# Optimization experiments

Measured on AMD Instinct MI355X. Metric: run time of the kernel, lower is better.

Reference implementation:

```python
import jax, jax.numpy as jnp
import numpy as np

BOND_D = 4    # disentangler bond dim (hard-coded 4 in torch init)
BOND_I = 16   # isometry bond dim (bond_dim kwarg)
F = 2         # feature_dim = 2*nCh, nCh=1 -> [x, 1-x] embedding
LEVELS = [128, 64, 32, 16, 8, 4]
NUM_CLASSES = 10
BATCH = 16


def setup_inputs() -> dict:
    key = jax.random.key(0)
    ks = iter(jax.random.split(key, 128))
    inp = {}
    inp["x"] = jax.random.uniform(next(ks), (BATCH, 1, 128, 128), dtype=jnp.float32)

    def mps_params(P, D, O):
        A = 0.2 * jax.random.normal(next(ks), (P, 4, F, D, D), dtype=jnp.float32)
        v = 0.2 * jax.random.normal(next(ks), (P, D), dtype=jnp.float32)
        w = 0.2 * jax.random.normal(next(ks), (P, D, O), dtype=jnp.float32)
        return A, v, w

    for l, H in enumerate(LEVELS, start=1):
        Pd = ((H - 2) // 2) ** 2   # number of disentangler patches
        Pi = (H // 2) ** 2         # number of isometry patches
        inp[f"d{l}A"], inp[f"d{l}v"], inp[f"d{l}w"] = mps_params(Pd, BOND_D, 4)
        inp[f"i{l}A"], inp[f"i{l}v"], inp[f"i{l}w"] = mps_params(Pi, BOND_I, 1)
    inp["fA"], inp["fv"], inp["fw"] = mps_params(1, BOND_I, NUM_CLASSES)
    return inp


def _patches(x):
    # x: [b, H, W] (H, W even) -> [b, (H/2)*(W/2), 4], same site order as
    # torch unfold(2,2,2).unfold(3,2,2).reshape(..., 4)
    b, H, W = x.shape
    return x.reshape(b, H // 2, 2, W // 2, 2).transpose(0, 1, 3, 2, 4).reshape(b, -1, 4)


def _unpatch(y, nh, nw):
    # y: [b, nh*nw, 4] -> [b, 2*nh, 2*nw], inverse spatial placement of 2x2 blocks
    b = y.shape[0]
    return y.reshape(b, nh, nw, 2, 2).transpose(0, 1, 3, 2, 4).reshape(b, 2 * nh, 2 * nw)


def _mps(patches, A, v, w):
    # Batched per-patch ReLU-MPS over 4 sites.
    # patches [b,P,4], A [P,4,F,D,D], v [P,D], w [P,D,O] -> [b,P,O]
    phi = jnp.stack([patches, 1.0 - patches], axis=-1)          # [b,P,4,F]
    M = jnp.einsum('bpsf,psfij->bpsij', phi, A)                 # [b,P,4,D,D]
    vec = jnp.einsum('pi,bpij->bpj', v, M[:, :, 0])             # [b,P,D]
    for s in range(1, 4):
        vec = jnp.einsum('bpi,bpij->bpj', vec, M[:, :, s])
    return jax.nn.relu(jnp.einsum('bpi,pio->bpo', vec, w))


def _level(x, dA, dv, dw, iA, iv, iw):
    # One MERA layer: disentangle shifted interior patches, write back, then
    # isometry-pool the full grid 2x2 -> 1.
    b, H, W = x.shape
    nh = (H - 2) // 2
    y = _mps(_patches(x[:, 1:-1, 1:-1]), dA, dv, dw)            # [b, nh*nh, 4]
    x = x.at[:, 1:-1, 1:-1].set(_unpatch(y, nh, nh))
    y2 = _mps(_patches(x), iA, iv, iw)                          # [b, (H/2)^2, 1]
    return y2.reshape(b, H // 2, W // 2)


def reference(x, d1A, d1v, d1w, i1A, i1v, i1w,
              d2A, d2v, d2w, i2A, i2v, i2w,
              d3A, d3v, d3w, i3A, i3v, i3w,
              d4A, d4v, d4w, i4A, i4v, i4w,
              d5A, d5v, d5w, i5A, i5v, i5w,
              d6A, d6v, d6w, i6A, i6v, i6w,
              fA, fv, fw):
    h = x[:, 0]  # nCh = 1
    levels = [(d1A, d1v, d1w, i1A, i1v, i1w), (d2A, d2v, d2w, i2A, i2v, i2w),
              (d3A, d3v, d3w, i3A, i3v, i3w), (d4A, d4v, d4w, i4A, i4v, i4w),
              (d5A, d5v, d5w, i5A, i5v, i5w), (d6A, d6v, d6w, i6A, i6v, i6w)]
    for p in levels:
        h = _level(h, *p)
    flat = h.reshape(h.shape[0], 1, 4)         # final 2x2 grid -> 4 sites
    return _mps(flat, fA, fv, fw)[:, 0]        # [b, NUM_CLASSES]
```

## Files before the change

### kernel.cpp

```cpp
#include <hip/hip_runtime.h>

#define BATCH 16

template <int CTRL>
__device__ __forceinline__ float qperm(float x) {
  int xi = __float_as_int(x);
  return __int_as_float(__builtin_amdgcn_update_dpp(xi, xi, CTRL, 0xF, 0xF, true));
}

__device__ __forceinline__ float4 f4fma(float s, float4 a, float4 c) {
  c.x = fmaf(s, a.x, c.x);
  c.y = fmaf(s, a.y, c.y);
  c.z = fmaf(s, a.z, c.z);
  c.w = fmaf(s, a.w, c.w);
  return c;
}

__device__ __forceinline__ void mps16_chain(const float* A, int jq,
                                            const float tt[4], float vec[4]) {
#pragma unroll
  for (int s = 0; s < 4; s++) {
    const float4* A0v = (const float4*)(A + s * 512) + jq;
    const float4* A1v = A0v + 64;
    float4 q0 = {0.f, 0.f, 0.f, 0.f}, q1 = {0.f, 0.f, 0.f, 0.f};
#define ISTEP(i)                                         \
  {                                                      \
    float sv = qperm<(((i) >> 2) * 0x55)>(vec[(i) & 3]); \
    q0 = f4fma(sv, A0v[(i) * 4], q0);                    \
    q1 = f4fma(sv, A1v[(i) * 4], q1);                    \
  }
    ISTEP(0) ISTEP(1) ISTEP(2) ISTEP(3)
    ISTEP(4) ISTEP(5) ISTEP(6) ISTEP(7)
    ISTEP(8) ISTEP(9) ISTEP(10) ISTEP(11)
    ISTEP(12) ISTEP(13) ISTEP(14) ISTEP(15)
#undef ISTEP
    float ph = tt[s], om = 1.0f - ph;
    vec[0] = ph * q0.x + om * q1.x;
    vec[1] = ph * q0.y + om * q1.y;
    vec[2] = ph * q0.z + om * q1.z;
    vec[3] = ph * q0.w + om * q1.w;
  }
}

template <int H, int XS>
__device__ __forceinline__ float fused_di_quad(
    const float* __restrict__ xb, int p, int jq,
    const float* __restrict__ dA, const float* __restrict__ dv,
    const float* __restrict__ dw,
    const float* __restrict__ iA, const float* __restrict__ iv,
    const float* __restrict__ iw) {
  constexpr int NH = (H - 2) / 2;
  constexpr int W2 = H / 2;
  int pi = p / W2, pj = p % W2;
  int r = 2 * pi + (jq >> 1), c = 2 * pj + (jq & 1);
  float tcell;
  bool border = (r == 0) | (r == H - 1) | (c == 0) | (c == H - 1);
  if (border) {
    tcell = xb[(r * H + c) * XS];
  } else {
    int dpi = (r - 1) >> 1, dpj = (c - 1) >> 1;
    int sd = ((r - 1) & 1) * 2 + ((c - 1) & 1);
    int dp = dpi * NH + dpj;
    int R0 = 1 + 2 * dpi, C0 = 1 + 2 * dpj;
    float tins[4];
    tins[0] = xb[(R0 * H + C0) * XS];
    tins[1] = xb[(R0 * H + C0 + 1) * XS];
    tins[2] = xb[((R0 + 1) * H + C0) * XS];
    tins[3] = xb[((R0 + 1) * H + C0 + 1) * XS];
    const float4* Av = (const float4*)(dA + dp * 128);
    float4 dvv = *(const float4*)(dv + dp * 4);
    float v0 = dvv.x, v1 = dvv.y, v2 = dvv.z, v3 = dvv.w;
#pragma unroll
    for (int s = 0; s < 4; s++) {
      const float4* A0 = Av + s * 8;
      float4 q0 = {0.f, 0.f, 0.f, 0.f}, q1 = {0.f, 0.f, 0.f, 0.f};
      q0 = f4fma(v0, A0[0], q0);
      q0 = f4fma(v1, A0[1], q0);
      q0 = f4fma(v2, A0[2], q0);
      q0 = f4fma(v3, A0[3], q0);
      q1 = f4fma(v0, A0[4], q1);
      q1 = f4fma(v1, A0[5], q1);
      q1 = f4fma(v2, A0[6], q1);
      q1 = f4fma(v3, A0[7], q1);
      float ph = tins[s], om = 1.0f - ph;
      v0 = ph * q0.x + om * q1.x;
      v1 = ph * q0.y + om * q1.y;
      v2 = ph * q0.z + om * q1.z;
      v3 = ph * q0.w + om * q1.w;
    }
    const float* wp = dw + dp * 16 + sd;
    float y = v0 * wp[0];
    y = fmaf(v1, wp[4], y);
    y = fmaf(v2, wp[8], y);
    y = fmaf(v3, wp[12], y);
    tcell = fmaxf(y, 0.0f);
  }
  float tt[4];
  tt[0] = qperm<0x00>(tcell);
  tt[1] = qperm<0x55>(tcell);
  tt[2] = qperm<0xAA>(tcell);
  tt[3] = qperm<0xFF>(tcell);
  float4 vv = *(const float4*)(iv + p * 16 + 4 * jq);
  float vec[4] = {vv.x, vv.y, vv.z, vv.w};
  mps16_chain(iA + (size_t)p * 2048, jq, tt, vec);
  float4 wv = *(const float4*)(iw + p * 16 + 4 * jq);
  float partial = vec[0] * wv.x;
  partial = fmaf(vec[1], wv.y, partial);
  partial = fmaf(vec[2], wv.z, partial);
  partial = fmaf(vec[3], wv.w, partial);
  partial += qperm<0xB1>(partial);
  partial += qperm<0x4E>(partial);
  return fmaxf(partial, 0.0f);
}

#define OFF_IA 0
#define OFF_IV 8192
#define OFF_IW 8256
#define OFF_DA 8320
#define OFF_DV 9640
#define OFF_DW 9680
#define LDS_TOT 9840

template <int H>
__global__ __launch_bounds__(256) void level_kernel(
    const float* __restrict__ xT, float* __restrict__ hn,
    const float* __restrict__ dA, const float* __restrict__ dv,
    const float* __restrict__ dw, const float* __restrict__ iA,
    const float* __restrict__ iv, const float* __restrict__ iw) {
  constexpr int W2 = H / 2, NH = (H - 2) / 2;
  __shared__ __align__(16) float lds[LDS_TOT];
  float4* l4 = (float4*)lds;
  const int tid = threadIdx.x;
  const int p0 = blockIdx.x * 4;
  const int pi = p0 / W2, pj0 = p0 % W2;
  const int jq = tid & 3, b = (tid >> 2) & 15, w = tid >> 6;
  const int pj = pj0 + w;
  const int r = 2 * pi + (jq >> 1), c = 2 * pj + (jq & 1);
  const bool border = (r == 0) | (r == H - 1) | (c == 0) | (c == H - 1);
  const int dpi = (r - 1) >> 1, dpj = (c - 1) >> 1;

  float xv0, xv1, xv2, xv3;
  if (border) {
    xv0 = xT[(r * H + c) * 16 + b];
  } else {
    int R0 = 1 + 2 * dpi, C0 = 1 + 2 * dpj;
    xv0 = xT[(R0 * H + C0) * 16 + b];
    xv1 = xT[(R0 * H + C0 + 1) * 16 + b];
    xv2 = xT[((R0 + 1) * H + C0) * 16 + b];
    xv3 = xT[((R0 + 1) * H + C0 + 1) * 16 + b];
  }

  {
    const float4* iA4 = (const float4*)iA + p0 * 512;
    float4 ra[8];
#pragma unroll
    for (int k = 0; k < 8; k++) ra[k] = iA4[tid + k * 256];

    float4 rd0, rd1;
    int sl0, gr0, sl1, gr1;
    const bool md1 = tid < 64;
    {
      int g = tid;
      int rs = g / 160, rem = g % 160, cs = rem / 32;
      gr0 = rem % 32;
      int di = min(max(pi - 1 + rs, 0), NH - 1);
      int dj = min(max(pj0 - 1 + cs, 0), NH - 1);
      sl0 = rs * 5 + cs;
      rd0 = *((const float4*)dA + (di * NH + dj) * 32 + gr0);
    }
    if (md1) {
      int g = tid + 256;
      int rs = g / 160, rem = g % 160, cs = rem / 32;
      gr1 = rem % 32;
      int di = min(max(pi - 1 + rs, 0), NH - 1);
      int dj = min(max(pj0 - 1 + cs, 0), NH - 1);
      sl1 = rs * 5 + cs;
      rd1 = *((const float4*)dA + (di * NH + dj) * 32 + gr1);
    }
    float4 rv;
    const bool mv = tid < 10;
    if (mv) {
      int rs = tid / 5, cs = tid % 5;
      int di = min(max(pi - 1 + rs, 0), NH - 1);
      int dj = min(max(pj0 - 1 + cs, 0), NH - 1);
      rv = *((const float4*)dv + (di * NH + dj));
    }
    float4 rw;
    const bool mw = tid < 40;
    if (mw) {
      int rs = tid / 20, rem = tid % 20, cs = rem / 4, gr = rem % 4;
      int di = min(max(pi - 1 + rs, 0), NH - 1);
      int dj = min(max(pj0 - 1 + cs, 0), NH - 1);
      rw = *((const float4*)dw + (di * NH + dj) * 4 + gr);
    }
    float4 rvv, rww;
    const bool mi = tid < 16;
    if (mi) {
      rvv = *((const float4*)iv + p0 * 4 + tid);
      rww = *((const float4*)iw + p0 * 4 + tid);
    }
#pragma unroll
    for (int k = 0; k < 8; k++) l4[OFF_IA / 4 + tid + k * 256] = ra[k];
    l4[OFF_DA / 4 + sl0 * 33 + gr0] = rd0;
    if (md1) l4[OFF_DA / 4 + sl1 * 33 + gr1] = rd1;
    if (mv) l4[OFF_DV / 4 + tid] = rv;
    if (mw) l4[OFF_DW / 4 + tid] = rw;
    if (mi) l4[OFF_IV / 4 + tid] = rvv;
    if (mi) l4[OFF_IW / 4 + tid] = rww;
  }
  __syncthreads();

  float tcell;
  if (border) {
    tcell = xv0;
  } else {
    int sd = ((r - 1) & 1) * 2 + ((c - 1) & 1);
    int slot = (dpi - pi + 1) * 5 + (dpj - pj0 + 1);
    const float4* Av = (const float4*)(lds + OFF_DA + slot * 132);
    float4 dvv = *(const float4*)(lds + OFF_DV + slot * 4);
    float v0 = dvv.x, v1 = dvv.y, v2 = dvv.z, v3 = dvv.w;
    float tins[4] = {xv0, xv1, xv2, xv3};
#pragma unroll
    for (int s = 0; s < 4; s++) {
      const float4* A0 = Av + s * 8;
      float4 q0 = {0.f, 0.f, 0.f, 0.f}, q1 = {0.f, 0.f, 0.f, 0.f};
      q0 = f4fma(v0, A0[0], q0);
      q0 = f4fma(v1, A0[1], q0);
      q0 = f4fma(v2, A0[2], q0);
      q0 = f4fma(v3, A0[3], q0);
      q1 = f4fma(v0, A0[4], q1);
      q1 = f4fma(v1, A0[5], q1);
      q1 = f4fma(v2, A0[6], q1);
      q1 = f4fma(v3, A0[7], q1);
      float ph = tins[s], om = 1.0f - ph;
      v0 = ph * q0.x + om * q1.x;
      v1 = ph * q0.y + om * q1.y;
      v2 = ph * q0.z + om * q1.z;
      v3 = ph * q0.w + om * q1.w;
    }
    const float* wp = lds + OFF_DW + slot * 16 + sd;
    float y = v0 * wp[0];
    y = fmaf(v1, wp[4], y);
    y = fmaf(v2, wp[8], y);
    y = fmaf(v3, wp[12], y);
    tcell = fmaxf(y, 0.0f);
  }
  float tt[4];
  tt[0] = qperm<0x00>(tcell);
  tt[1] = qperm<0x55>(tcell);
  tt[2] = qperm<0xAA>(tcell);
  tt[3] = qperm<0xFF>(tcell);
  float4 vv = *(const float4*)(lds + OFF_IV + w * 16 + 4 * jq);
  float vec[4] = {vv.x, vv.y, vv.z, vv.w};
  mps16_chain(lds + OFF_IA + w * 2048, jq, tt, vec);
  float4 wv = *(const float4*)(lds + OFF_IW + w * 16 + 4 * jq);
  float partial = vec[0] * wv.x;
  partial = fmaf(vec[1], wv.y, partial);
  partial = fmaf(vec[2], wv.z, partial);
  partial = fmaf(vec[3], wv.w, partial);
  partial += qperm<0xB1>(partial);
  partial += qperm<0x4E>(partial);
  if (jq == 0) hn[(p0 + w) * 16 + b] = fmaxf(partial, 0.0f);
}

__global__ __launch_bounds__(256) void transpose_kernel(
    const float* __restrict__ x, float* __restrict__ xT) {
  __shared__ float t[64][17];
  int tid = threadIdx.x;
  int c0 = blockIdx.x * 64;
  {
    int bb = tid >> 4, c4 = tid & 15;
    float4 v = *((const float4*)(x + bb * 16384 + c0) + c4);
    t[c4 * 4 + 0][bb] = v.x;
    t[c4 * 4 + 1][bb] = v.y;
    t[c4 * 4 + 2][bb] = v.z;
    t[c4 * 4 + 3][bb] = v.w;
  }
  __syncthreads();
  {
    int cl = tid >> 2, bq = tid & 3;
    float4 v;
    v.x = t[cl][bq * 4 + 0];
    v.y = t[cl][bq * 4 + 1];
    v.z = t[cl][bq * 4 + 2];
    v.w = t[cl][bq * 4 + 3];
    *((float4*)(xT + (c0 + cl) * 16) + bq) = v;
  }
}

struct TailArgs {
  const float* h4;
  const float* in[15];
  float* out;
};

__global__ __launch_bounds__(256) void tail2_kernel(TailArgs a) {
  __shared__ float h5l[4][16];
  __shared__ float h6l[4][4];
  int tid = threadIdx.x;
  {
    int jq = tid & 3, p = (tid >> 2) & 15, bl = tid >> 6;
    int b = blockIdx.x * 4 + bl;
    float o = fused_di_quad<8, 16>(a.h4 + b, p, jq, a.in[0], a.in[1], a.in[2],
                                   a.in[3], a.in[4], a.in[5]);
    if (jq == 0) h5l[bl][p] = o;
  }
  __syncthreads();
  if (tid < 64) {
    int jq = tid & 3, p = (tid >> 2) & 3, bl = tid >> 4;
    float o = fused_di_quad<4, 1>(&h5l[bl][0], p, jq, a.in[6], a.in[7],
                                  a.in[8], a.in[9], a.in[10], a.in[11]);
    if (jq == 0) h6l[bl][p] = o;
  }
  __syncthreads();
  if (tid < 16) {
    int jq = tid & 3, bl = tid >> 2;
    const float* fA = a.in[12];
    const float* fv = a.in[13];
    const float* fw = a.in[14];
    float tt[4] = {h6l[bl][0], h6l[bl][1], h6l[bl][2], h6l[bl][3]};
    float4 vv = *(const float4*)(fv + 4 * jq);
    float vec[4] = {vv.x, vv.y, vv.z, vv.w};
    mps16_chain(fA, jq, tt, vec);
    float acc[10];
#pragma unroll
    for (int o = 0; o < 10; o++) acc[o] = 0.f;
#pragma unroll
    for (int k = 0; k < 4; k++)
#pragma unroll
      for (int o = 0; o < 10; o++)
        acc[o] = fmaf(vec[k], fw[(4 * jq + k) * 10 + o], acc[o]);
#pragma unroll
    for (int o = 0; o < 10; o++) {
      acc[o] += qperm<0xB1>(acc[o]);
      acc[o] += qperm<0x4E>(acc[o]);
    }
    if (jq == 0) {
      int b = blockIdx.x * 4 + bl;
#pragma unroll
      for (int o = 0; o < 10; o++) a.out[b * 10 + o] = fmaxf(acc[o], 0.0f);
    }
  }
}

extern "C" void kernel_launch(void* const* d_in, const int* in_sizes, int n_in,
                              void* d_out, int out_size, void* d_ws, size_t ws_size,
                              hipStream_t stream) {
  const float* x = (const float*)d_in[0];
  float* ws = (float*)d_ws;
  float* xT = ws;
  float* h1 = xT + 262144;
  float* h2 = h1 + 65536;
  float* h3 = h2 + 16384;
  float* h4 = h3 + 4096;

  transpose_kernel<<<256, 256, 0, stream>>>(x, xT);
  level_kernel<128><<<1024, 256, 0, stream>>>(
      xT, h1, (const float*)d_in[1], (const float*)d_in[2],
      (const float*)d_in[3], (const float*)d_in[4], (const float*)d_in[5],
      (const float*)d_in[6]);
  level_kernel<64><<<256, 256, 0, stream>>>(
      h1, h2, (const float*)d_in[7], (const float*)d_in[8],
      (const float*)d_in[9], (const float*)d_in[10], (const float*)d_in[11],
      (const float*)d_in[12]);
  level_kernel<32><<<64, 256, 0, stream>>>(
      h2, h3, (const float*)d_in[13], (const float*)d_in[14],
      (const float*)d_in[15], (const float*)d_in[16], (const float*)d_in[17],
      (const float*)d_in[18]);
  level_kernel<16><<<16, 256, 0, stream>>>(
      h3, h4, (const float*)d_in[19], (const float*)d_in[20],
      (const float*)d_in[21], (const float*)d_in[22], (const float*)d_in[23],
      (const float*)d_in[24]);

  TailArgs ta;
  ta.h4 = h4;
  for (int i = 0; i < 15; i++) ta.in[i] = (const float*)d_in[25 + i];
  ta.out = (float*)d_out;
  tail2_kernel<<<4, 256, 0, stream>>>(ta);
}
```

Before: 195.5 us.

## Fuse all MERA levels into one cooperative persistent kernel with grid syncs

Replaces the transpose kernel, four per-level kernels and the tail kernel with one cooperative kernel of 512 blocks that runs each level as a phase separated by grid.sync. Level 1 reads the raw input layout directly, which drops the transpose pass, and each block handles two patch groups. Level 5 moves out of the tail into its own phase, and the tail stages its weights in LDS inside a single block. This removes per-launch overhead and inter-kernel gaps, at the cost of grid-wide barriers, idle blocks in the late phases, and uncoalesced strided reads of the raw input in level 1.

```diff
diff --git a/kernel.cpp b/kernel.cpp
--- a/kernel.cpp
+++ b/kernel.cpp
@@ -1,4 +1,7 @@
 #include <hip/hip_runtime.h>
+#include <hip/hip_cooperative_groups.h>
+
+namespace cg = cooperative_groups;
 
 #define BATCH 16
 
@@ -44,11 +47,8 @@
 
 template <int H, int XS>
 __device__ __forceinline__ float fused_di_quad(
-    const float* __restrict__ xb, int p, int jq,
-    const float* __restrict__ dA, const float* __restrict__ dv,
-    const float* __restrict__ dw,
-    const float* __restrict__ iA, const float* __restrict__ iv,
-    const float* __restrict__ iw) {
+    const float* xb, int p, int jq, const float* dA, const float* dv,
+    const float* dw, const float* iA, const float* iv, const float* iw) {
   constexpr int NH = (H - 2) / 2;
   constexpr int W2 = H / 2;
   int pi = p / W2, pj = p % W2;
@@ -120,18 +120,21 @@
 #define OFF_DV 9640
 #define OFF_DW 9680
 #define LDS_TOT 9840
-
-template <int H>
-__global__ __launch_bounds__(256) void level_kernel(
-    const float* __restrict__ xT, float* __restrict__ hn,
-    const float* __restrict__ dA, const float* __restrict__ dv,
-    const float* __restrict__ dw, const float* __restrict__ iA,
-    const float* __restrict__ iv, const float* __restrict__ iw) {
+#define OFF_X6 (OFF_DA + 264)
+#define OFF_H6 (OFF_DA + 1056)
+
+template <int H, bool RAW>
+__device__ void level_phase(float* lds, const float* __restrict__ xin,
+                            float* __restrict__ hn,
+                            const float* __restrict__ dA,
+                            const float* __restrict__ dv,
+                            const float* __restrict__ dw,
+                            const float* __restrict__ iA,
+                            const float* __restrict__ iv,
+                            const float* __restrict__ iw, int p0) {
   constexpr int W2 = H / 2, NH = (H - 2) / 2;
-  __shared__ __align__(16) float lds[LDS_TOT];
   float4* l4 = (float4*)lds;
   const int tid = threadIdx.x;
-  const int p0 = blockIdx.x * 4;
   const int pi = p0 / W2, pj0 = p0 % W2;
   const int jq = tid & 3, b = (tid >> 2) & 15, w = tid >> 6;
   const int pj = pj0 + w;
@@ -140,15 +143,30 @@
   const int dpi = (r - 1) >> 1, dpj = (c - 1) >> 1;
 
   float xv0, xv1, xv2, xv3;
-  if (border) {
-    xv0 = xT[(r * H + c) * 16 + b];
+  if (RAW) {
+    const float* xb = xin + b * H * H;
+    if (border) {
+      xv0 = xb[r * H + c];
+    } else {
+      int R0 = 1 + 2 * dpi, C0 = 1 + 2 * dpj;
+      xv0 = xb[R0 * H + C0];
+      xv1 = xb[R0 * H + C0 + 1];
+      xv2 = xb[(R0 + 1) * H + C0];
+      xv3 = xb[(R0 + 1) * H + C0 + 1];
+    }
   } else {
-    int R0 = 1 + 2 * dpi, C0 = 1 + 2 * dpj;
-    xv0 = xT[(R0 * H + C0) * 16 + b];
-    xv1 = xT[(R0 * H + C0 + 1) * 16 + b];
-    xv2 = xT[((R0 + 1) * H + C0) * 16 + b];
-    xv3 = xT[((R0 + 1) * H + C0 + 1) * 16 + b];
-  }
+    if (border) {
+      xv0 = xin[(r * H + c) * 16 + b];
+    } else {
+      int R0 = 1 + 2 * dpi, C0 = 1 + 2 * dpj;
+      xv0 = xin[(R0 * H + C0) * 16 + b];
+      xv1 = xin[(R0 * H + C0 + 1) * 16 + b];
+      xv2 = xin[((R0 + 1) * H + C0) * 16 + b];
+      xv3 = xin[((R0 + 1) * H + C0 + 1) * 16 + b];
+    }
+  }
+
+  __syncthreads();
 
   {
     const float4* iA4 = (const float4*)iA + p0 * 512;
@@ -263,65 +281,85 @@
   if (jq == 0) hn[(p0 + w) * 16 + b] = fmaxf(partial, 0.0f);
 }
 
-__global__ __launch_bounds__(256) void transpose_kernel(
-    const float* __restrict__ x, float* __restrict__ xT) {
-  __shared__ float t[64][17];
-  int tid = threadIdx.x;
-  int c0 = blockIdx.x * 64;
-  {
-    int bb = tid >> 4, c4 = tid & 15;
-    float4 v = *((const float4*)(x + bb * 16384 + c0) + c4);
-    t[c4 * 4 + 0][bb] = v.x;
-    t[c4 * 4 + 1][bb] = v.y;
-    t[c4 * 4 + 2][bb] = v.z;
-    t[c4 * 4 + 3][bb] = v.w;
-  }
-  __syncthreads();
-  {
-    int cl = tid >> 2, bq = tid & 3;
-    float4 v;
-    v.x = t[cl][bq * 4 + 0];
-    v.y = t[cl][bq * 4 + 1];
-    v.z = t[cl][bq * 4 + 2];
-    v.w = t[cl][bq * 4 + 3];
-    *((float4*)(xT + (c0 + cl) * 16) + bq) = v;
-  }
-}
-
-struct TailArgs {
-  const float* h4;
-  const float* in[15];
+struct MegaArgs {
+  const float* x;
+  const float* P[39];
+  float* h1;
+  float* h2;
+  float* h3;
+  float* h4;
+  float* h5;
   float* out;
 };
 
-__global__ __launch_bounds__(256) void tail2_kernel(TailArgs a) {
-  __shared__ float h5l[4][16];
-  __shared__ float h6l[4][4];
-  int tid = threadIdx.x;
+__device__ void tail_phase(float* lds, const MegaArgs& a) {
+  float4* l4 = (float4*)lds;
+  const int tid = threadIdx.x;
+  const float* d6A = a.P[30];
+  const float* d6v = a.P[31];
+  const float* d6w = a.P[32];
+  const float* i6A = a.P[33];
+  const float* i6v = a.P[34];
+  const float* i6w = a.P[35];
+  const float* fA = a.P[36];
+  const float* fv = a.P[37];
+  const float* fw = a.P[38];
+  __syncthreads();
   {
-    int jq = tid & 3, p = (tid >> 2) & 15, bl = tid >> 6;
-    int b = blockIdx.x * 4 + bl;
-    float o = fused_di_quad<8, 16>(a.h4 + b, p, jq, a.in[0], a.in[1], a.in[2],
-                                   a.in[3], a.in[4], a.in[5]);
-    if (jq == 0) h5l[bl][p] = o;
+    const float4* g = (const float4*)i6A;
+    float4 ra[8];
+#pragma unroll
+    for (int k = 0; k < 8; k++) ra[k] = g[tid + k * 256];
+    float4 rdA;
+    const bool mA = tid < 32;
+    if (mA) rdA = ((const float4*)d6A)[tid];
+    float4 rdv;
+    const bool mdv = tid == 0;
+    if (mdv) rdv = ((const float4*)d6v)[0];
+    float4 rdw;
+    const bool mdw = tid < 4;
+    if (mdw) rdw = ((const float4*)d6w)[tid];
+    float4 riv, riw;
+    const bool mi = tid < 16;
+    if (mi) {
+      riv = ((const float4*)i6v)[tid];
+      riw = ((const float4*)i6w)[tid];
+    }
+    float x6v = a.h5[(tid & 15) * 16 + (tid >> 4)];
+#pragma unroll
+    for (int k = 0; k < 8; k++) l4[OFF_IA / 4 + tid + k * 256] = ra[k];
+    if (mA) l4[OFF_DA / 4 + tid] = rdA;
+    if (mdv) l4[OFF_DV / 4] = rdv;
+    if (mdw) l4[OFF_DW / 4 + tid] = rdw;
+    if (mi) {
+      l4[OFF_IV / 4 + tid] = riv;
+      l4[OFF_IW / 4 + tid] = riw;
+    }
+    lds[OFF_X6 + tid] = x6v;
+  }
+  __syncthreads();
+  {
+    int jq = tid & 3, p = (tid >> 2) & 3, b = tid >> 4;
+    float o = fused_di_quad<4, 1>(lds + OFF_X6 + b * 16, p, jq, lds + OFF_DA,
+                                  lds + OFF_DV, lds + OFF_DW, lds + OFF_IA,
+                                  lds + OFF_IV, lds + OFF_IW);
+    if (jq == 0) lds[OFF_H6 + b * 4 + p] = o;
+  }
+  __syncthreads();
+  {
+    const float4* g = (const float4*)fA;
+    float4 r0 = g[tid], r1 = g[tid + 256];
+    l4[OFF_IA / 4 + tid] = r0;
+    l4[OFF_IA / 4 + tid + 256] = r1;
   }
   __syncthreads();
   if (tid < 64) {
-    int jq = tid & 3, p = (tid >> 2) & 3, bl = tid >> 4;
-    float o = fused_di_quad<4, 1>(&h5l[bl][0], p, jq, a.in[6], a.in[7],
-                                  a.in[8], a.in[9], a.in[10], a.in[11]);
-    if (jq == 0) h6l[bl][p] = o;
-  }
-  __syncthreads();
-  if (tid < 16) {
-    int jq = tid & 3, bl = tid >> 2;
-    const float* fA = a.in[12];
-    const float* fv = a.in[13];
-    const float* fw = a.in[14];
-    float tt[4] = {h6l[bl][0], h6l[bl][1], h6l[bl][2], h6l[bl][3]};
+    int jq = tid & 3, b = tid >> 2;
+    float tt[4] = {lds[OFF_H6 + b * 4 + 0], lds[OFF_H6 + b * 4 + 1],
+                   lds[OFF_H6 + b * 4 + 2], lds[OFF_H6 + b * 4 + 3]};
     float4 vv = *(const float4*)(fv + 4 * jq);
     float vec[4] = {vv.x, vv.y, vv.z, vv.w};
-    mps16_chain(fA, jq, tt, vec);
+    mps16_chain(lds + OFF_IA, jq, tt, vec);
     float acc[10];
 #pragma unroll
     for (int o = 0; o < 10; o++) acc[o] = 0.f;
@@ -336,45 +374,54 @@
       acc[o] += qperm<0x4E>(acc[o]);
     }
     if (jq == 0) {
-      int b = blockIdx.x * 4 + bl;
 #pragma unroll
       for (int o = 0; o < 10; o++) a.out[b * 10 + o] = fmaxf(acc[o], 0.0f);
     }
   }
 }
 
+#define LPARAMS(l)                                                    \
+  a.P[6 * ((l)-1) + 0], a.P[6 * ((l)-1) + 1], a.P[6 * ((l)-1) + 2],   \
+      a.P[6 * ((l)-1) + 3], a.P[6 * ((l)-1) + 4], a.P[6 * ((l)-1) + 5]
+
+__global__ __launch_bounds__(256) void mega_kernel(MegaArgs a) {
+  __shared__ __align__(16) float lds[LDS_TOT];
+  cg::grid_group grid = cg::this_grid();
+  const int bid = blockIdx.x;
+
+  level_phase<128, true>(lds, a.x, a.h1, LPARAMS(1), bid * 8);
+  level_phase<128, true>(lds, a.x, a.h1, LPARAMS(1), bid * 8 + 4);
+  __threadfence();
+  grid.sync();
+  if (bid < 256) level_phase<64, false>(lds, a.h1, a.h2, LPARAMS(2), bid * 4);
+  __threadfence();
+  grid.sync();
+  if (bid < 64) level_phase<32, false>(lds, a.h2, a.h3, LPARAMS(3), bid * 4);
+  __threadfence();
+  grid.sync();
+  if (bid < 16) level_phase<16, false>(lds, a.h3, a.h4, LPARAMS(4), bid * 4);
+  __threadfence();
+  grid.sync();
+  if (bid < 4) level_phase<8, false>(lds, a.h4, a.h5, LPARAMS(5), bid * 4);
+  __threadfence();
+  grid.sync();
+  if (bid == 0) tail_phase(lds, a);
+}
+
 extern "C" void kernel_launch(void* const* d_in, const int* in_sizes, int n_in,
-                              void* d_out, int out_size, void* d_ws, size_t ws_size,
-                              hipStream_t stream) {
-  const float* x = (const float*)d_in[0];
+                              void* d_out, int out_size, void* d_ws,
+                              size_t ws_size, hipStream_t stream) {
+  MegaArgs ma;
+  ma.x = (const float*)d_in[0];
+  for (int i = 0; i < 39; i++) ma.P[i] = (const float*)d_in[1 + i];
   float* ws = (float*)d_ws;
-  float* xT = ws;
-  float* h1 = xT + 262144;
-  float* h2 = h1 + 65536;
-  float* h3 = h2 + 16384;
-  float* h4 = h3 + 4096;
-
-  transpose_kernel<<<256, 256, 0, stream>>>(x, xT);
-  level_kernel<128><<<1024, 256, 0, stream>>>(
-      xT, h1, (const float*)d_in[1], (const float*)d_in[2],
-      (const float*)d_in[3], (const float*)d_in[4], (const float*)d_in[5],
-      (const float*)d_in[6]);
-  level_kernel<64><<<256, 256, 0, stream>>>(
-      h1, h2, (const float*)d_in[7], (const float*)d_in[8],
-      (const float*)d_in[9], (const float*)d_in[10], (const float*)d_in[11],
-      (const float*)d_in[12]);
-  level_kernel<32><<<64, 256, 0, stream>>>(
-      h2, h3, (const float*)d_in[13], (const float*)d_in[14],
-      (const float*)d_in[15], (const float*)d_in[16], (const float*)d_in[17],
-      (const float*)d_in[18]);
-  level_kernel<16><<<16, 256, 0, stream>>>(
-      h3, h4, (const float*)d_in[19], (const float*)d_in[20],
-      (const float*)d_in[21], (const float*)d_in[22], (const float*)d_in[23],
-      (const float*)d_in[24]);
-
-  TailArgs ta;
-  ta.h4 = h4;
-  for (int i = 0; i < 15; i++) ta.in[i] = (const float*)d_in[25 + i];
-  ta.out = (float*)d_out;
-  tail2_kernel<<<4, 256, 0, stream>>>(ta);
-}
+  ma.h1 = ws;
+  ma.h2 = ma.h1 + 65536;
+  ma.h3 = ma.h2 + 16384;
+  ma.h4 = ma.h3 + 4096;
+  ma.h5 = ma.h4 + 1024;
+  ma.out = (float*)d_out;
+  void* args[] = {&ma};
+  hipLaunchCooperativeKernel(reinterpret_cast<void*>(mega_kernel), dim3(512),
+                             dim3(256), args, 0, stream);
+}
```

Result: slower. 685.4 us (+250.5%).

## Split tail into level-5 kernel and single-block smem-staged level-6 tail

Applied to the files above, without the earlier changes.

Level 5 now runs on the generic level_kernel, writing a new h5 workspace buffer. Level 6 and the final MPS move into a single-block tail kernel that first stages all level-6 and final weights and the activations into shared memory with wide, coalesced loads, then runs the contractions from LDS. The aim is to replace scattered dependent global reads of weights in the serial tail with one bulk prefetch. The cost is an extra kernel launch, one more global round trip for h5, and the tail running on a single block.

```diff
diff --git a/kernel.cpp b/kernel.cpp
--- a/kernel.cpp
+++ b/kernel.cpp
@@ -44,11 +44,8 @@
 
 template <int H, int XS>
 __device__ __forceinline__ float fused_di_quad(
-    const float* __restrict__ xb, int p, int jq,
-    const float* __restrict__ dA, const float* __restrict__ dv,
-    const float* __restrict__ dw,
-    const float* __restrict__ iA, const float* __restrict__ iv,
-    const float* __restrict__ iw) {
+    const float* xb, int p, int jq, const float* dA, const float* dv,
+    const float* dw, const float* iA, const float* iv, const float* iw) {
   constexpr int NH = (H - 2) / 2;
   constexpr int W2 = H / 2;
   int pi = p / W2, pj = p % W2;
@@ -288,40 +285,75 @@
   }
 }
 
-struct TailArgs {
-  const float* h4;
-  const float* in[15];
+struct Tail6Args {
+  const float* h5;
+  const float* in[9];
   float* out;
 };
 
-__global__ __launch_bounds__(256) void tail2_kernel(TailArgs a) {
-  __shared__ float h5l[4][16];
-  __shared__ float h6l[4][4];
-  int tid = threadIdx.x;
+__global__ __launch_bounds__(256) void tail6_kernel(Tail6Args a) {
+  __shared__ __align__(16) float s_i6A[8192];
+  __shared__ __align__(16) float s_fA[2048];
+  __shared__ __align__(16) float s_d6A[128];
+  __shared__ __align__(16) float s_d6v[4];
+  __shared__ __align__(16) float s_d6w[16];
+  __shared__ __align__(16) float s_i6v[64];
+  __shared__ __align__(16) float s_i6w[64];
+  __shared__ float s_x6[256];
+  __shared__ float s_h6[64];
+  const int tid = threadIdx.x;
   {
-    int jq = tid & 3, p = (tid >> 2) & 15, bl = tid >> 6;
-    int b = blockIdx.x * 4 + bl;
-    float o = fused_di_quad<8, 16>(a.h4 + b, p, jq, a.in[0], a.in[1], a.in[2],
-                                   a.in[3], a.in[4], a.in[5]);
-    if (jq == 0) h5l[bl][p] = o;
+    const float4* g = (const float4*)a.in[3];
+    float4 ra[8];
+#pragma unroll
+    for (int k = 0; k < 8; k++) ra[k] = g[tid + k * 256];
+    const float4* gf = (const float4*)a.in[6];
+    float4 rf0 = gf[tid], rf1 = gf[tid + 256];
+    float4 rdA;
+    const bool mA = tid < 32;
+    if (mA) rdA = ((const float4*)a.in[0])[tid];
+    float4 rdv;
+    if (tid == 0) rdv = ((const float4*)a.in[1])[0];
+    float4 rdw;
+    const bool mdw = tid < 4;
+    if (mdw) rdw = ((const float4*)a.in[2])[tid];
+    float4 riv, riw;
+    const bool mi = tid < 16;
+    if (mi) {
+      riv = ((const float4*)a.in[4])[tid];
+      riw = ((const float4*)a.in[5])[tid];
+    }
+    float xv = a.h5[tid];
+#pragma unroll
+    for (int k = 0; k < 8; k++) ((float4*)s_i6A)[tid + k * 256] = ra[k];
+    ((float4*)s_fA)[tid] = rf0;
+    ((float4*)s_fA)[tid + 256] = rf1;
+    if (mA) ((float4*)s_d6A)[tid] = rdA;
+    if (tid == 0) ((float4*)s_d6v)[0] = rdv;
+    if (mdw) ((float4*)s_d6w)[tid] = rdw;
+    if (mi) {
+      ((float4*)s_i6v)[tid] = riv;
+      ((float4*)s_i6w)[tid] = riw;
+    }
+    s_x6[(tid & 15) * 16 + (tid >> 4)] = xv;
+  }
+  __syncthreads();
+  {
+    int jq = tid & 3, p = (tid >> 2) & 3, b = tid >> 4;
+    float o = fused_di_quad<4, 1>(s_x6 + b * 16, p, jq, s_d6A, s_d6v, s_d6w,
+                                  s_i6A, s_i6v, s_i6w);
+    if (jq == 0) s_h6[b * 4 + p] = o;
   }
   __syncthreads();
   if (tid < 64) {
-    int jq = tid & 3, p = (tid >> 2) & 3, bl = tid >> 4;
-    float o = fused_di_quad<4, 1>(&h5l[bl][0], p, jq, a.in[6], a.in[7],
-                                  a.in[8], a.in[9], a.in[10], a.in[11]);
-    if (jq == 0) h6l[bl][p] = o;
-  }
-  __syncthreads();
-  if (tid < 16) {
-    int jq = tid & 3, bl = tid >> 2;
-    const float* fA = a.in[12];
-    const float* fv = a.in[13];
-    const float* fw = a.in[14];
-    float tt[4] = {h6l[bl][0], h6l[bl][1], h6l[bl][2], h6l[bl][3]};
+    int jq = tid & 3, b = tid >> 2;
+    const float* fv = a.in[7];
+    const float* fw = a.in[8];
+    float tt[4] = {s_h6[b * 4 + 0], s_h6[b * 4 + 1], s_h6[b * 4 + 2],
+                   s_h6[b * 4 + 3]};
     float4 vv = *(const float4*)(fv + 4 * jq);
     float vec[4] = {vv.x, vv.y, vv.z, vv.w};
-    mps16_chain(fA, jq, tt, vec);
+    mps16_chain(s_fA, jq, tt, vec);
     float acc[10];
 #pragma unroll
     for (int o = 0; o < 10; o++) acc[o] = 0.f;
@@ -336,7 +368,6 @@
       acc[o] += qperm<0x4E>(acc[o]);
     }
     if (jq == 0) {
-      int b = blockIdx.x * 4 + bl;
 #pragma unroll
       for (int o = 0; o < 10; o++) a.out[b * 10 + o] = fmaxf(acc[o], 0.0f);
     }
@@ -344,8 +375,8 @@
 }
 
 extern "C" void kernel_launch(void* const* d_in, const int* in_sizes, int n_in,
-                              void* d_out, int out_size, void* d_ws, size_t ws_size,
-                              hipStream_t stream) {
+                              void* d_out, int out_size, void* d_ws,
+                              size_t ws_size, hipStream_t stream) {
   const float* x = (const float*)d_in[0];
   float* ws = (float*)d_ws;
   float* xT = ws;
@@ -353,6 +384,7 @@
   float* h2 = h1 + 65536;
   float* h3 = h2 + 16384;
   float* h4 = h3 + 4096;
+  float* h5 = h4 + 1024;
 
   transpose_kernel<<<256, 256, 0, stream>>>(x, xT);
   level_kernel<128><<<1024, 256, 0, stream>>>(
@@ -371,10 +403,13 @@
       h3, h4, (const float*)d_in[19], (const float*)d_in[20],
       (const float*)d_in[21], (const float*)d_in[22], (const float*)d_in[23],
       (const float*)d_in[24]);
-
-  TailArgs ta;
-  ta.h4 = h4;
-  for (int i = 0; i < 15; i++) ta.in[i] = (const float*)d_in[25 + i];
+  level_kernel<8><<<4, 256, 0, stream>>>(
+      h4, h5, (const float*)d_in[25], (const float*)d_in[26],
+      (const float*)d_in[27], (const float*)d_in[28], (const float*)d_in[29],
+      (const float*)d_in[30]);
+  Tail6Args ta;
+  ta.h5 = h5;
+  for (int i = 0; i < 9; i++) ta.in[i] = (const float*)d_in[31 + i];
   ta.out = (float*)d_out;
-  tail2_kernel<<<4, 256, 0, stream>>>(ta);
-}
+  tail6_kernel<<<1, 256, 0, stream>>>(ta);
+}
```

Result: no change. 198.0 us, median of 2 (+1.3%).

## Drop transpose kernel, use batch-major layout, and fuse level 4 into tail

Applied to the files above, without the earlier changes.

The level kernels now read the input in its native batch-major layout, so the separate transpose pass and its workspace round-trip go away. Outputs are staged in LDS and written as float4 per batch row. Level 4 is folded into a per-batch tail kernel that runs levels 4-6 and the final MPS, which removes two launches. The cost is uncoalesced strided reads across batches in the level kernels, and a tail of only 16 blocks with idle threads in its later stages.

```diff
diff --git a/kernel.cpp b/kernel.cpp
--- a/kernel.cpp
+++ b/kernel.cpp
@@ -42,13 +42,10 @@
   }
 }
 
-template <int H, int XS>
+template <int H>
 __device__ __forceinline__ float fused_di_quad(
-    const float* __restrict__ xb, int p, int jq,
-    const float* __restrict__ dA, const float* __restrict__ dv,
-    const float* __restrict__ dw,
-    const float* __restrict__ iA, const float* __restrict__ iv,
-    const float* __restrict__ iw) {
+    const float* xb, int p, int jq, const float* dA, const float* dv,
+    const float* dw, const float* iA, const float* iv, const float* iw) {
   constexpr int NH = (H - 2) / 2;
   constexpr int W2 = H / 2;
   int pi = p / W2, pj = p % W2;
@@ -56,17 +53,17 @@
   float tcell;
   bool border = (r == 0) | (r == H - 1) | (c == 0) | (c == H - 1);
   if (border) {
-    tcell = xb[(r * H + c) * XS];
+    tcell = xb[r * H + c];
   } else {
     int dpi = (r - 1) >> 1, dpj = (c - 1) >> 1;
     int sd = ((r - 1) & 1) * 2 + ((c - 1) & 1);
     int dp = dpi * NH + dpj;
     int R0 = 1 + 2 * dpi, C0 = 1 + 2 * dpj;
     float tins[4];
-    tins[0] = xb[(R0 * H + C0) * XS];
-    tins[1] = xb[(R0 * H + C0 + 1) * XS];
-    tins[2] = xb[((R0 + 1) * H + C0) * XS];
-    tins[3] = xb[((R0 + 1) * H + C0 + 1) * XS];
+    tins[0] = xb[R0 * H + C0];
+    tins[1] = xb[R0 * H + C0 + 1];
+    tins[2] = xb[(R0 + 1) * H + C0];
+    tins[3] = xb[(R0 + 1) * H + C0 + 1];
     const float4* Av = (const float4*)(dA + dp * 128);
     float4 dvv = *(const float4*)(dv + dp * 4);
     float v0 = dvv.x, v1 = dvv.y, v2 = dvv.z, v3 = dvv.w;
@@ -123,12 +120,13 @@
 
 template <int H>
 __global__ __launch_bounds__(256) void level_kernel(
-    const float* __restrict__ xT, float* __restrict__ hn,
+    const float* __restrict__ xin, float* __restrict__ hn,
     const float* __restrict__ dA, const float* __restrict__ dv,
     const float* __restrict__ dw, const float* __restrict__ iA,
     const float* __restrict__ iv, const float* __restrict__ iw) {
   constexpr int W2 = H / 2, NH = (H - 2) / 2;
   __shared__ __align__(16) float lds[LDS_TOT];
+  __shared__ __align__(16) float s_out[64];
   float4* l4 = (float4*)lds;
   const int tid = threadIdx.x;
   const int p0 = blockIdx.x * 4;
@@ -138,16 +136,17 @@
   const int r = 2 * pi + (jq >> 1), c = 2 * pj + (jq & 1);
   const bool border = (r == 0) | (r == H - 1) | (c == 0) | (c == H - 1);
   const int dpi = (r - 1) >> 1, dpj = (c - 1) >> 1;
+  const float* xb = xin + b * (H * H);
 
   float xv0, xv1, xv2, xv3;
   if (border) {
-    xv0 = xT[(r * H + c) * 16 + b];
+    xv0 = xb[r * H + c];
   } else {
     int R0 = 1 + 2 * dpi, C0 = 1 + 2 * dpj;
-    xv0 = xT[(R0 * H + C0) * 16 + b];
-    xv1 = xT[(R0 * H + C0 + 1) * 16 + b];
-    xv2 = xT[((R0 + 1) * H + C0) * 16 + b];
-    xv3 = xT[((R0 + 1) * H + C0 + 1) * 16 + b];
+    xv0 = xb[R0 * H + C0];
+    xv1 = xb[R0 * H + C0 + 1];
+    xv2 = xb[(R0 + 1) * H + C0];
+    xv3 = xb[(R0 + 1) * H + C0 + 1];
   }
 
   {
@@ -260,65 +259,56 @@
   partial = fmaf(vec[3], wv.w, partial);
   partial += qperm<0xB1>(partial);
   partial += qperm<0x4E>(partial);
-  if (jq == 0) hn[(p0 + w) * 16 + b] = fmaxf(partial, 0.0f);
-}
-
-__global__ __launch_bounds__(256) void transpose_kernel(
-    const float* __restrict__ x, float* __restrict__ xT) {
-  __shared__ float t[64][17];
-  int tid = threadIdx.x;
-  int c0 = blockIdx.x * 64;
-  {
-    int bb = tid >> 4, c4 = tid & 15;
-    float4 v = *((const float4*)(x + bb * 16384 + c0) + c4);
-    t[c4 * 4 + 0][bb] = v.x;
-    t[c4 * 4 + 1][bb] = v.y;
-    t[c4 * 4 + 2][bb] = v.z;
-    t[c4 * 4 + 3][bb] = v.w;
-  }
-  __syncthreads();
-  {
-    int cl = tid >> 2, bq = tid & 3;
-    float4 v;
-    v.x = t[cl][bq * 4 + 0];
-    v.y = t[cl][bq * 4 + 1];
-    v.z = t[cl][bq * 4 + 2];
-    v.w = t[cl][bq * 4 + 3];
-    *((float4*)(xT + (c0 + cl) * 16) + bq) = v;
-  }
-}
-
-struct TailArgs {
-  const float* h4;
-  const float* in[15];
+  if (jq == 0) s_out[b * 4 + w] = fmaxf(partial, 0.0f);
+  __syncthreads();
+  if (tid < 16) {
+    float4 v = *(const float4*)(s_out + tid * 4);
+    *(float4*)(hn + tid * (W2 * W2) + p0) = v;
+  }
+}
+
+struct Tail4Args {
+  const float* h3;
+  const float* in[21];
   float* out;
 };
 
-__global__ __launch_bounds__(256) void tail2_kernel(TailArgs a) {
-  __shared__ float h5l[4][16];
-  __shared__ float h6l[4][4];
-  int tid = threadIdx.x;
+__global__ __launch_bounds__(256) void tail4_kernel(Tail4Args a) {
+  __shared__ float x4[256];
+  __shared__ float x5[64];
+  __shared__ float x6[16];
+  __shared__ float h6[4];
+  const int b = blockIdx.x;
+  const int tid = threadIdx.x;
+  x4[tid] = a.h3[b * 256 + tid];
+  __syncthreads();
   {
-    int jq = tid & 3, p = (tid >> 2) & 15, bl = tid >> 6;
-    int b = blockIdx.x * 4 + bl;
-    float o = fused_di_quad<8, 16>(a.h4 + b, p, jq, a.in[0], a.in[1], a.in[2],
-                                   a.in[3], a.in[4], a.in[5]);
-    if (jq == 0) h5l[bl][p] = o;
+    int jq = tid & 3, p = tid >> 2;
+    float o = fused_di_quad<16>(x4, p, jq, a.in[0], a.in[1], a.in[2],
+                                a.in[3], a.in[4], a.in[5]);
+    if (jq == 0) x5[p] = o;
   }
   __syncthreads();
   if (tid < 64) {
-    int jq = tid & 3, p = (tid >> 2) & 3, bl = tid >> 4;
-    float o = fused_di_quad<4, 1>(&h5l[bl][0], p, jq, a.in[6], a.in[7],
-                                  a.in[8], a.in[9], a.in[10], a.in[11]);
-    if (jq == 0) h6l[bl][p] = o;
+    int jq = tid & 3, p = tid >> 2;
+    float o = fused_di_quad<8>(x5, p, jq, a.in[6], a.in[7], a.in[8],
+                               a.in[9], a.in[10], a.in[11]);
+    if (jq == 0) x6[p] = o;
   }
   __syncthreads();
   if (tid < 16) {
-    int jq = tid & 3, bl = tid >> 2;
-    const float* fA = a.in[12];
-    const float* fv = a.in[13];
-    const float* fw = a.in[14];
-    float tt[4] = {h6l[bl][0], h6l[bl][1], h6l[bl][2], h6l[bl][3]};
+    int jq = tid & 3, p = tid >> 2;
+    float o = fused_di_quad<4>(x6, p, jq, a.in[12], a.in[13], a.in[14],
+                               a.in[15], a.in[16], a.in[17]);
+    if (jq == 0) h6[p] = o;
+  }
+  __syncthreads();
+  if (tid < 4) {
+    int jq = tid;
+    const float* fA = a.in[18];
+    const float* fv = a.in[19];
+    const float* fw = a.in[20];
+    float tt[4] = {h6[0], h6[1], h6[2], h6[3]};
     float4 vv = *(const float4*)(fv + 4 * jq);
     float vec[4] = {vv.x, vv.y, vv.z, vv.w};
     mps16_chain(fA, jq, tt, vec);
@@ -336,7 +326,6 @@
       acc[o] += qperm<0x4E>(acc[o]);
     }
     if (jq == 0) {
-      int b = blockIdx.x * 4 + bl;
 #pragma unroll
       for (int o = 0; o < 10; o++) a.out[b * 10 + o] = fmaxf(acc[o], 0.0f);
     }
@@ -344,19 +333,16 @@
 }
 
 extern "C" void kernel_launch(void* const* d_in, const int* in_sizes, int n_in,
-                              void* d_out, int out_size, void* d_ws, size_t ws_size,
-                              hipStream_t stream) {
+                              void* d_out, int out_size, void* d_ws,
+                              size_t ws_size, hipStream_t stream) {
   const float* x = (const float*)d_in[0];
   float* ws = (float*)d_ws;
-  float* xT = ws;
-  float* h1 = xT + 262144;
+  float* h1 = ws;
   float* h2 = h1 + 65536;
   float* h3 = h2 + 16384;
-  float* h4 = h3 + 4096;
-
-  transpose_kernel<<<256, 256, 0, stream>>>(x, xT);
+
   level_kernel<128><<<1024, 256, 0, stream>>>(
-      xT, h1, (const float*)d_in[1], (const float*)d_in[2],
+      x, h1, (const float*)d_in[1], (const float*)d_in[2],
       (const float*)d_in[3], (const float*)d_in[4], (const float*)d_in[5],
       (const float*)d_in[6]);
   level_kernel<64><<<256, 256, 0, stream>>>(
@@ -367,14 +353,9 @@
       h2, h3, (const float*)d_in[13], (const float*)d_in[14],
       (const float*)d_in[15], (const float*)d_in[16], (const float*)d_in[17],
       (const float*)d_in[18]);
-  level_kernel<16><<<16, 256, 0, stream>>>(
-      h3, h4, (const float*)d_in[19], (const float*)d_in[20],
-      (const float*)d_in[21], (const float*)d_in[22], (const float*)d_in[23],
-      (const float*)d_in[24]);
-
-  TailArgs ta;
-  ta.h4 = h4;
-  for (int i = 0; i < 15; i++) ta.in[i] = (const float*)d_in[25 + i];
+  Tail4Args ta;
+  ta.h3 = h3;
+  for (int i = 0; i < 21; i++) ta.in[i] = (const float*)d_in[19 + i];
   ta.out = (float*)d_out;
-  tail2_kernel<<<4, 256, 0, stream>>>(ta);
-}
+  tail4_kernel<<<BATCH, 256, 0, stream>>>(ta);
+}
```

After: 199.2 us. About the same (+1.9%).
